# Performance work log

Hardware: AMD Instinct MI355X
Metric: run time of the kernel (lower is better)

The kernel has to match this reference:

```python
import jax, jax.numpy as jnp
import numpy as np
from math import sqrt

SEQ, NIN, NH, NOUT, HEADS = 4096, 1024, 128, 1024, 8
DOUT = HEADS * (2 * NH + NOUT)  # 10240
EPS = 1e-5

def setup_inputs() -> dict:
    key = jax.random.key(0)
    k1, k2, k3 = jax.random.split(key, 3)
    x = jax.random.normal(k1, (SEQ, NIN), dtype=jnp.float32)
    W = jax.random.normal(k2, (DOUT, NIN), dtype=jnp.float32) * (1.0 / sqrt(NIN))
    b = jax.random.normal(k3, (DOUT,), dtype=jnp.float32) * 0.01
    ln_w = jnp.ones((NOUT,), dtype=jnp.float32)
    ln_b = jnp.zeros((NOUT,), dtype=jnp.float32)
    return {"x": x, "W": W, "b": b, "ln_w": ln_w, "ln_b": ln_b}

def reference(x, W, b, ln_w, ln_b):
    # fused QKV projection: (S, NIN) -> (S, HEADS, 2*NH + NOUT)
    out = (x @ W.T + b).reshape(x.shape[0], HEADS, -1)
    keys, queries, values = jnp.split(out, (NH, 2 * NH), axis=-1)
    keys = keys / sqrt(keys.shape[-1])
    # logits[i, j, h] = sum_k keys[i,h,k] * queries[j,h,k]
    logits = jnp.einsum('ihk,jhk->ijh', keys, queries)
    attention = jax.nn.softmax(logits, axis=1)
    # sum over j and heads -> (S, NOUT)
    output = jnp.einsum('ijh,jhe->ie', attention, values)
    # LayerNorm over last dim, elementwise affine, eps=1e-5
    mean = jnp.mean(output, axis=-1, keepdims=True)
    var = jnp.var(output, axis=-1, keepdims=True)
    normed = (output - mean) / jnp.sqrt(var + EPS)
    return normed * ln_w + ln_b
```

## Files before the change

### kernel.cpp

```cpp
#include <hip/hip_runtime.h>

typedef __attribute__((ext_vector_type(8))) __bf16 bf16x8;
typedef __attribute__((ext_vector_type(4))) __bf16 bf16x4;
typedef __attribute__((ext_vector_type(4))) float f32x4;
typedef __attribute__((ext_vector_type(16))) float f32x16;

#define SEQ   4096
#define NIN   1024
#define DH    128
#define NOUTD 1024
#define HEADS 8
#define CPH   1280
#define L2E   1.44269504f

static __device__ inline f32x16 zero16() {
  f32x16 z;
#pragma unroll
  for (int r = 0; r < 16; ++r) z[r] = 0.f;
  return z;
}

static __device__ inline unsigned pk2(float a, float b) {
  unsigned short ua = __builtin_bit_cast(unsigned short, (__bf16)a);
  unsigned short ub = __builtin_bit_cast(unsigned short, (__bf16)b);
  return (unsigned)ua | ((unsigned)ub << 16);
}

__global__ __launch_bounds__(256) void k_cvt(const float* __restrict__ src,
                                             __bf16* __restrict__ dst, int n) {
  int i = (blockIdx.x * 256 + threadIdx.x) * 4;
  if (i >= n) return;
  float4 v = *(const float4*)(src + i);
  bf16x4 o = { (__bf16)v.x, (__bf16)v.y, (__bf16)v.z, (__bf16)v.w };
  *(bf16x4*)(dst + i) = o;
}

__global__ __launch_bounds__(256) void k_zero(float4* __restrict__ p) {
  p[(size_t)blockIdx.x * 256 + threadIdx.x] = float4{0.f, 0.f, 0.f, 0.f};
}

__global__ __launch_bounds__(256) void k_gemm_qkv(
    const __bf16* __restrict__ xb, const __bf16* __restrict__ wb,
    const float* __restrict__ bias,
    __bf16* __restrict__ Kx, __bf16* __restrict__ Q2, __bf16* __restrict__ V2)
{
  __shared__ __align__(16) __bf16 As[128 * 32];
  __shared__ __align__(16) __bf16 Bs[128 * 32];
  const int tid = threadIdx.x;
  const int w = tid >> 6, l = tid & 63;
  const int i0 = blockIdx.x * 128;
  const int n0 = blockIdx.y * 128;
  const int lrow = l & 15;
  const int lkb  = (l >> 4) * 16;
  const int soff = (w * 2) * 1024 + l * 16;

  f32x4 acc[4][4] = {};

  for (int kt = 0; kt < 32; ++kt) {
    __syncthreads();
#pragma unroll
    for (int q = 0; q < 2; ++q) {
      int off = soff + q * 1024;
      int row = off >> 6, kb = off & 63;
      const __bf16* ga = xb + (size_t)(i0 + row) * NIN + kt * 32 + (kb >> 1);
      const __bf16* gb = wb + (size_t)(n0 + row) * NIN + kt * 32 + (kb >> 1);
      __builtin_amdgcn_global_load_lds(
          (const __attribute__((address_space(1))) void*)ga,
          (__attribute__((address_space(3))) void*)((char*)As + (w * 2 + q) * 1024),
          16, 0, 0);
      __builtin_amdgcn_global_load_lds(
          (const __attribute__((address_space(1))) void*)gb,
          (__attribute__((address_space(3))) void*)((char*)Bs + (w * 2 + q) * 1024),
          16, 0, 0);
    }
    __syncthreads();
    bf16x8 af[4], bfr[4];
#pragma unroll
    for (int mi = 0; mi < 4; ++mi)
      af[mi] = *(const bf16x8*)((const char*)As + (((w >> 1) * 64 + mi * 16 + lrow) * 64) + lkb);
#pragma unroll
    for (int ni = 0; ni < 4; ++ni)
      bfr[ni] = *(const bf16x8*)((const char*)Bs + (((w & 1) * 64 + ni * 16 + lrow) * 64) + lkb);
#pragma unroll
    for (int mi = 0; mi < 4; ++mi)
#pragma unroll
      for (int ni = 0; ni < 4; ++ni)
        acc[mi][ni] = __builtin_amdgcn_mfma_f32_16x16x32_bf16(af[mi], bfr[ni], acc[mi][ni], 0, 0, 0);
  }

  const int iw = i0 + (w >> 1) * 64;
  const int nw = n0 + (w & 1) * 64;
  const int lhi = l >> 4;
#pragma unroll
  for (int ni = 0; ni < 4; ++ni) {
    int n = nw + ni * 16 + lrow;
    float bv = bias[n];
    int h = n / CPH;
    int c = n - h * CPH;
    if (c < 128) {
#pragma unroll
      for (int mi = 0; mi < 4; ++mi)
#pragma unroll
        for (int r = 0; r < 4; ++r) {
          int i = iw + mi * 16 + lhi * 4 + r;
          float v = acc[mi][ni][r] + bv;
          Kx[(((size_t)h * SEQ + i) << 7) + c] = (__bf16)(v * 0.08838834764831845f);
        }
    } else if (c < 256) {
      int d = c - 128;
      size_t qEl = ((size_t)(h * 16 + (d >> 3)) << 15) + (size_t)(d & 7);
#pragma unroll
      for (int mi = 0; mi < 4; ++mi)
#pragma unroll
        for (int r = 0; r < 4; ++r) {
          int j = iw + mi * 16 + lhi * 4 + r;
          Q2[qEl + ((size_t)j << 3)] = (__bf16)(acc[mi][ni][r] + bv);
        }
    } else {
      int e = c - 256;
#pragma unroll
      for (int mi = 0; mi < 4; ++mi) {
        int jb = iw + mi * 16 + lhi * 4;
        int J = jb >> 3, js = jb & 7;
        size_t vEl = (((size_t)(h * 512 + J)) << 13) + ((size_t)e << 3) + js;
        bf16x4 pk = { (__bf16)(acc[mi][ni][0] + bv), (__bf16)(acc[mi][ni][1] + bv),
                      (__bf16)(acc[mi][ni][2] + bv), (__bf16)(acc[mi][ni][3] + bv) };
        *(bf16x4*)(V2 + vEl) = pk;
      }
    }
  }
}

__global__ __launch_bounds__(256) void k_stats(
    const __bf16* __restrict__ Kx, const __bf16* __restrict__ Q2,
    float* __restrict__ stat_m, float* __restrict__ stat_il)
{
  __shared__ __align__(16) char Qb[2][16384];
  const int tid = threadIdx.x;
  const int w = tid >> 6, l = tid & 63;
  const int l31 = l & 31, hl = l >> 5;
  const int b = blockIdx.x;
  const int h = b >> 5;
  const int i_base = (b & 31) * 128;
  const __bf16* Kh = Kx + ((size_t)h * SEQ << 7);
  const char* q2b = (const char*)Q2 + ((size_t)h << 20);

  bf16x8 kf[8];
#pragma unroll
  for (int c = 0; c < 8; ++c)
    kf[c] = *(const bf16x8*)(Kh + (((size_t)(i_base + 32 * w + l31)) << 7) + c * 16 + hl * 8);

  float m_run = -1e30f, l_run = 0.f;

#pragma unroll
  for (int k = 0; k < 4; ++k) {
    int s = tid + k * 256;
    const char* src = q2b + ((size_t)(s >> 6) << 16) + (size_t)(s & 63) * 16;
    __builtin_amdgcn_global_load_lds(
        (const __attribute__((address_space(1))) void*)src,
        (__attribute__((address_space(3))) void*)(Qb[0] + s * 16), 16, 0, 0);
  }
  __syncthreads();

  for (int jt = 0; jt < 64; ++jt) {
    const int cur = jt & 1;
    if (jt < 63) {
      int j0n = (jt + 1) * 64;
#pragma unroll
      for (int k = 0; k < 4; ++k) {
        int s = tid + k * 256;
        const char* src = q2b + ((size_t)(s >> 6) << 16) + (size_t)(j0n + (s & 63)) * 16;
        __builtin_amdgcn_global_load_lds(
            (const __attribute__((address_space(1))) void*)src,
            (__attribute__((address_space(3))) void*)(Qb[cur ^ 1] + s * 16), 16, 0, 0);
      }
    }
    const char* qb = Qb[cur];

    f32x16 s0 = zero16(), s1 = zero16();
#pragma unroll
    for (int c = 0; c < 8; ++c) {
      bf16x8 a0 = *(const bf16x8*)(qb + (((2 * c + hl) * 64 + l31) << 4));
      bf16x8 a1 = *(const bf16x8*)(qb + (((2 * c + hl) * 64 + 32 + l31) << 4));
      s0 = __builtin_amdgcn_mfma_f32_32x32x16_bf16(a0, kf[c], s0, 0, 0, 0);
      s1 = __builtin_amdgcn_mfma_f32_32x32x16_bf16(a1, kf[c], s1, 0, 0, 0);
    }

    float pm = -1e30f;
#pragma unroll
    for (int r = 0; r < 16; ++r) pm = fmaxf(pm, fmaxf(s0[r], s1[r]));
    float mn = fmaxf(m_run, pm);
    l_run *= exp2f((m_run - mn) * L2E);
    float a = 0.f;
#pragma unroll
    for (int r = 0; r < 16; ++r)
      a += exp2f((s0[r] - mn) * L2E) + exp2f((s1[r] - mn) * L2E);
    l_run += a;
    m_run = mn;
    __syncthreads();
  }

  float mp = __shfl_xor(m_run, 32);
  float lp = __shfl_xor(l_run, 32);
  float mf = fmaxf(m_run, mp);
  float lf = l_run * exp2f((m_run - mf) * L2E) + lp * exp2f((mp - mf) * L2E);
  if (hl == 0) {
    int i = i_base + 32 * w + l31;
    stat_m[h * SEQ + i] = mf;
    stat_il[h * SEQ + i] = 1.0f / lf;
  }
}

__global__ __launch_bounds__(512, 2) void k_attn3(
    const __bf16* __restrict__ Kx, const __bf16* __restrict__ Q2,
    const __bf16* __restrict__ V2, const float* __restrict__ stat_m,
    const float* __restrict__ stat_il, float* __restrict__ out)
{
  __shared__ __align__(16) char Qb[2][8192];
  __shared__ __align__(16) char Vb[2][16384];
  __shared__ float s_linv[256];

  const int tid = threadIdx.x;
  const int w = tid >> 6, l = tid & 63;
  const int l31 = l & 31, hl = l >> 5;
  const int islot = w & 3, eslot = w >> 2;

  const int b = blockIdx.x;
  const int et = b & 3;
  const int h = ((b >> 2) & 1) + 2 * (b >> 7);
  const int it = (b >> 3) & 15;
  const int i_base = it * 256, e_base = et * 256;

  const __bf16* Kh = Kx + ((size_t)h * SEQ << 7);
  const char* q2b = (const char*)Q2 + ((size_t)h << 20);
  const char* v2b = (const char*)V2 + ((size_t)(h * 512) << 14) + ((size_t)e_base << 4);

  if (tid < 256) s_linv[tid] = stat_il[h * SEQ + i_base + tid];
  const int iw0 = i_base + islot * 64;
  const float m0 = stat_m[h * SEQ + iw0 + l31];
  const float m1 = stat_m[h * SEQ + iw0 + 32 + l31];

  bf16x8 kf[2][8];
#pragma unroll
  for (int ig = 0; ig < 2; ++ig)
#pragma unroll
    for (int c = 0; c < 8; ++c)
      kf[ig][c] = *(const bf16x8*)(Kh + (((size_t)(iw0 + ig * 32 + l31)) << 7) + c * 16 + hl * 8);

  f32x16 acc[2][4];
#pragma unroll
  for (int ig = 0; ig < 2; ++ig)
#pragma unroll
    for (int n = 0; n < 4; ++n) acc[ig][n] = zero16();

  {
    const char* srcQ = q2b + ((size_t)(tid >> 5) << 16) + (size_t)(tid & 31) * 16;
    __builtin_amdgcn_global_load_lds(
        (const __attribute__((address_space(1))) void*)srcQ,
        (__attribute__((address_space(3))) void*)(Qb[0] + tid * 16), 16, 0, 0);
#pragma unroll
    for (int k = 0; k < 2; ++k) {
      int s = tid + k * 512;
      const char* srcV = v2b + ((size_t)(s >> 8) << 14) + (size_t)(s & 255) * 16;
      __builtin_amdgcn_global_load_lds(
          (const __attribute__((address_space(1))) void*)srcV,
          (__attribute__((address_space(3))) void*)(Vb[0] + s * 16), 16, 0, 0);
    }
  }
  __syncthreads();

  for (int jt = 0; jt < 128; ++jt) {
    const int cur = jt & 1;
    if (jt < 127) {
      const int j0n = (jt + 1) * 32;
      const char* srcQ = q2b + ((size_t)(tid >> 5) << 16) + (size_t)(j0n + (tid & 31)) * 16;
      __builtin_amdgcn_global_load_lds(
          (const __attribute__((address_space(1))) void*)srcQ,
          (__attribute__((address_space(3))) void*)(Qb[cur ^ 1] + tid * 16), 16, 0, 0);
#pragma unroll
      for (int k = 0; k < 2; ++k) {
        int s = tid + k * 512;
        const char* srcV = v2b + ((size_t)((jt + 1) * 4 + (s >> 8)) << 14) + (size_t)(s & 255) * 16;
        __builtin_amdgcn_global_load_lds(
            (const __attribute__((address_space(1))) void*)srcV,
            (__attribute__((address_space(3))) void*)(Vb[cur ^ 1] + s * 16), 16, 0, 0);
      }
    }
    const char* qb = Qb[cur];
    const char* vb = Vb[cur];

    f32x16 s0 = zero16(), s1 = zero16();
#pragma unroll
    for (int c = 0; c < 8; ++c) {
      bf16x8 a0 = *(const bf16x8*)(qb + (((2 * c + hl) * 32 + l31) << 4));
      s0 = __builtin_amdgcn_mfma_f32_32x32x16_bf16(a0, kf[0][c], s0, 0, 0, 0);
      s1 = __builtin_amdgcn_mfma_f32_32x32x16_bf16(a0, kf[1][c], s1, 0, 0, 0);
    }

    bf16x8 pf[2][2];
#pragma unroll
    for (int ig = 0; ig < 2; ++ig) {
      const f32x16& sv = ig ? s1 : s0;
      const float mi = ig ? m1 : m0;
#pragma unroll
      for (int c2 = 0; c2 < 2; ++c2) {
        const int base = 8 * c2;
        float e0 = exp2f((sv[base + 0] - mi) * L2E);
        float e1 = exp2f((sv[base + 1] - mi) * L2E);
        float e2 = exp2f((sv[base + 2] - mi) * L2E);
        float e3 = exp2f((sv[base + 3] - mi) * L2E);
        float e4 = exp2f((sv[base + 4] - mi) * L2E);
        float e5 = exp2f((sv[base + 5] - mi) * L2E);
        float e6 = exp2f((sv[base + 6] - mi) * L2E);
        float e7 = exp2f((sv[base + 7] - mi) * L2E);
        unsigned WA0 = pk2(e0, e1), WA1 = pk2(e2, e3);
        unsigned WB0 = pk2(e4, e5), WB1 = pk2(e6, e7);
        unsigned send0 = hl ? WA0 : WB0;
        unsigned send1 = hl ? WA1 : WB1;
        unsigned r0 = (unsigned)__shfl_xor((int)send0, 32);
        unsigned r1 = (unsigned)__shfl_xor((int)send1, 32);
        int4 qd;
        qd.x = (int)(hl ? r0 : WA0);
        qd.y = (int)(hl ? r1 : WA1);
        qd.z = (int)(hl ? WB0 : r0);
        qd.w = (int)(hl ? WB1 : r1);
        pf[ig][c2] = __builtin_bit_cast(bf16x8, qd);
      }
    }

#pragma unroll
    for (int c2 = 0; c2 < 2; ++c2)
#pragma unroll
      for (int n = 0; n < 4; ++n) {
        bf16x8 bv = *(const bf16x8*)(vb + (((2 * c2 + hl) * 256 + eslot * 128 + 32 * n + l31) << 4));
        acc[0][n] = __builtin_amdgcn_mfma_f32_32x32x16_bf16(pf[0][c2], bv, acc[0][n], 0, 0, 0);
        acc[1][n] = __builtin_amdgcn_mfma_f32_32x32x16_bf16(pf[1][c2], bv, acc[1][n], 0, 0, 0);
      }
    __syncthreads();
  }

#pragma unroll
  for (int ig = 0; ig < 2; ++ig)
#pragma unroll
    for (int n = 0; n < 4; ++n) {
      const int e = e_base + eslot * 128 + 32 * n + l31;
#pragma unroll
      for (int r = 0; r < 16; ++r) {
        int row = (r & 3) + 8 * (r >> 2) + 4 * hl;
        int iloc = islot * 64 + ig * 32 + row;
        float v = acc[ig][n][r] * s_linv[iloc];
        atomicAdd(out + (((size_t)(i_base + iloc)) << 10) + e, v);
      }
    }
}

__global__ __launch_bounds__(256) void k_ln(float* __restrict__ io,
                                            const float* __restrict__ lw,
                                            const float* __restrict__ lb) {
  const int i = blockIdx.x, t = threadIdx.x;
  const int w = t >> 6, l = t & 63;
  float4 v = *(const float4*)(io + ((size_t)i << 10) + t * 4);
  float s = v.x + v.y + v.z + v.w;
  float q = v.x * v.x + v.y * v.y + v.z * v.z + v.w * v.w;
#pragma unroll
  for (int d = 1; d < 64; d <<= 1) {
    s += __shfl_xor(s, d);
    q += __shfl_xor(q, d);
  }
  __shared__ float red[4][2];
  if (l == 0) { red[w][0] = s; red[w][1] = q; }
  __syncthreads();
  s = red[0][0] + red[1][0] + red[2][0] + red[3][0];
  q = red[0][1] + red[1][1] + red[2][1] + red[3][1];
  float mean = s * (1.0f / 1024.0f);
  float var = q * (1.0f / 1024.0f) - mean * mean;
  float rstd = rsqrtf(var + 1e-5f);
  float4 gw = *(const float4*)(lw + t * 4);
  float4 gb = *(const float4*)(lb + t * 4);
  float4 ov;
  ov.x = (v.x - mean) * rstd * gw.x + gb.x;
  ov.y = (v.y - mean) * rstd * gw.y + gb.y;
  ov.z = (v.z - mean) * rstd * gw.z + gb.z;
  ov.w = (v.w - mean) * rstd * gw.w + gb.w;
  *(float4*)(io + ((size_t)i << 10) + t * 4) = ov;
}

extern "C" void kernel_launch(void* const* d_in, const int* in_sizes, int n_in,
                              void* d_out, int out_size, void* d_ws, size_t ws_size,
                              hipStream_t stream) {
  (void)in_sizes; (void)n_in; (void)out_size; (void)ws_size;
  const float* x  = (const float*)d_in[0];
  const float* W  = (const float*)d_in[1];
  const float* b  = (const float*)d_in[2];
  const float* lw = (const float*)d_in[3];
  const float* lb = (const float*)d_in[4];
  float* out = (float*)d_out;
  char* ws = (char*)d_ws;

  __bf16* xb = (__bf16*)ws;
  __bf16* wb = (__bf16*)(ws + (size_t)8  * 1024 * 1024);
  __bf16* Kx = (__bf16*)(ws + (size_t)28 * 1024 * 1024);
  __bf16* Q2 = (__bf16*)(ws + (size_t)36 * 1024 * 1024);
  __bf16* V2 = (__bf16*)(ws + (size_t)44 * 1024 * 1024);
  float* stat_m  = (float*)ws;
  float* stat_il = (float*)(ws + (size_t)128 * 1024);

  k_cvt<<<4096, 256, 0, stream>>>(x, xb, SEQ * NIN);
  k_cvt<<<10240, 256, 0, stream>>>(W, wb, HEADS * CPH * NIN);
  k_gemm_qkv<<<dim3(32, 80), 256, 0, stream>>>(xb, wb, b, Kx, Q2, V2);
  k_zero<<<4096, 256, 0, stream>>>((float4*)out);
  k_stats<<<256, 256, 0, stream>>>(Kx, Q2, stat_m, stat_il);
  k_attn3<<<512, 512, 0, stream>>>(Kx, Q2, V2, stat_m, stat_il, out);
  k_ln<<<4096, 256, 0, stream>>>(out, lw, lb);
}
```

Measured before the change: 1.011 ms.

## Materialize normalized attention matrix and compute output with a single large GEMM

Measured after the change: 1.012 ms. Within noise of the previous version (+0.1%).

```diff
diff --git a/kernel.cpp b/kernel.cpp
--- a/kernel.cpp
+++ b/kernel.cpp
@@ -12,6 +12,7 @@
 #define HEADS 8
 #define CPH   1280
 #define L2E   1.44269504f
+#define KTOT  32768
 
 static __device__ inline f32x16 zero16() {
   f32x16 z;
@@ -42,7 +43,8 @@
 __global__ __launch_bounds__(256) void k_gemm_qkv(
     const __bf16* __restrict__ xb, const __bf16* __restrict__ wb,
     const float* __restrict__ bias,
-    __bf16* __restrict__ Kx, __bf16* __restrict__ Q2, __bf16* __restrict__ V2)
+    __bf16* __restrict__ Kx, __bf16* __restrict__ Q2, __bf16* __restrict__ Vd,
+    int vmode)
 {
   __shared__ __align__(16) __bf16 As[128 * 32];
   __shared__ __align__(16) __bf16 Bs[128 * 32];
@@ -118,14 +120,18 @@
         }
     } else {
       int e = c - 256;
+      bf16x4 pk = { (__bf16)(acc[0][ni][0]), (__bf16)(0.f), (__bf16)(0.f), (__bf16)(0.f) };
 #pragma unroll
       for (int mi = 0; mi < 4; ++mi) {
         int jb = iw + mi * 16 + lhi * 4;
-        int J = jb >> 3, js = jb & 7;
-        size_t vEl = (((size_t)(h * 512 + J)) << 13) + ((size_t)e << 3) + js;
-        bf16x4 pk = { (__bf16)(acc[mi][ni][0] + bv), (__bf16)(acc[mi][ni][1] + bv),
-                      (__bf16)(acc[mi][ni][2] + bv), (__bf16)(acc[mi][ni][3] + bv) };
-        *(bf16x4*)(V2 + vEl) = pk;
+        pk = bf16x4{ (__bf16)(acc[mi][ni][0] + bv), (__bf16)(acc[mi][ni][1] + bv),
+                     (__bf16)(acc[mi][ni][2] + bv), (__bf16)(acc[mi][ni][3] + bv) };
+        if (vmode) {
+          *(bf16x4*)(Vd + (size_t)e * KTOT + (size_t)h * SEQ + jb) = pk;
+        } else {
+          int J = jb >> 3, js = jb & 7;
+          *(bf16x4*)(Vd + (((size_t)(h * 512 + J)) << 13) + ((size_t)e << 3) + js) = pk;
+        }
       }
     }
   }
@@ -208,6 +214,158 @@
     int i = i_base + 32 * w + l31;
     stat_m[h * SEQ + i] = mf;
     stat_il[h * SEQ + i] = 1.0f / lf;
+  }
+}
+
+__global__ __launch_bounds__(256) void k_pwrite(
+    const __bf16* __restrict__ Kx, const __bf16* __restrict__ Q2,
+    const float* __restrict__ stat_m, const float* __restrict__ stat_il,
+    __bf16* __restrict__ P)
+{
+  __shared__ __align__(16) char Qb[2][16384];
+  const int tid = threadIdx.x;
+  const int w = tid >> 6, l = tid & 63;
+  const int l31 = l & 31, hl = l >> 5;
+  const int b = blockIdx.x;
+  const int h = b >> 5;
+  const int i_base = (b & 31) * 128;
+  const __bf16* Kh = Kx + ((size_t)h * SEQ << 7);
+  const char* q2b = (const char*)Q2 + ((size_t)h << 20);
+
+  const int i = i_base + 32 * w + l31;
+  const float m_i = stat_m[h * SEQ + i];
+  const float il_i = stat_il[h * SEQ + i];
+  __bf16* prow = P + ((size_t)i << 15) + (size_t)h * SEQ;
+
+  bf16x8 kf[8];
+#pragma unroll
+  for (int c = 0; c < 8; ++c)
+    kf[c] = *(const bf16x8*)(Kh + (((size_t)i) << 7) + c * 16 + hl * 8);
+
+#pragma unroll
+  for (int k = 0; k < 4; ++k) {
+    int s = tid + k * 256;
+    const char* src = q2b + ((size_t)(s >> 6) << 16) + (size_t)(s & 63) * 16;
+    __builtin_amdgcn_global_load_lds(
+        (const __attribute__((address_space(1))) void*)src,
+        (__attribute__((address_space(3))) void*)(Qb[0] + s * 16), 16, 0, 0);
+  }
+  __syncthreads();
+
+  for (int jt = 0; jt < 64; ++jt) {
+    const int cur = jt & 1;
+    if (jt < 63) {
+      int j0n = (jt + 1) * 64;
+#pragma unroll
+      for (int k = 0; k < 4; ++k) {
+        int s = tid + k * 256;
+        const char* src = q2b + ((size_t)(s >> 6) << 16) + (size_t)(j0n + (s & 63)) * 16;
+        __builtin_amdgcn_global_load_lds(
+            (const __attribute__((address_space(1))) void*)src,
+            (__attribute__((address_space(3))) void*)(Qb[cur ^ 1] + s * 16), 16, 0, 0);
+      }
+    }
+    const char* qb = Qb[cur];
+
+    f32x16 s0 = zero16(), s1 = zero16();
+#pragma unroll
+    for (int c = 0; c < 8; ++c) {
+      bf16x8 a0 = *(const bf16x8*)(qb + (((2 * c + hl) * 64 + l31) << 4));
+      bf16x8 a1 = *(const bf16x8*)(qb + (((2 * c + hl) * 64 + 32 + l31) << 4));
+      s0 = __builtin_amdgcn_mfma_f32_32x32x16_bf16(a0, kf[c], s0, 0, 0, 0);
+      s1 = __builtin_amdgcn_mfma_f32_32x32x16_bf16(a1, kf[c], s1, 0, 0, 0);
+    }
+
+#pragma unroll
+    for (int c2 = 0; c2 < 4; ++c2) {
+      const f32x16& sv = (c2 >> 1) ? s1 : s0;
+      const int base = (c2 & 1) * 8;
+      float e0 = il_i * exp2f((sv[base + 0] - m_i) * L2E);
+      float e1 = il_i * exp2f((sv[base + 1] - m_i) * L2E);
+      float e2 = il_i * exp2f((sv[base + 2] - m_i) * L2E);
+      float e3 = il_i * exp2f((sv[base + 3] - m_i) * L2E);
+      float e4 = il_i * exp2f((sv[base + 4] - m_i) * L2E);
+      float e5 = il_i * exp2f((sv[base + 5] - m_i) * L2E);
+      float e6 = il_i * exp2f((sv[base + 6] - m_i) * L2E);
+      float e7 = il_i * exp2f((sv[base + 7] - m_i) * L2E);
+      unsigned WA0 = pk2(e0, e1), WA1 = pk2(e2, e3);
+      unsigned WB0 = pk2(e4, e5), WB1 = pk2(e6, e7);
+      unsigned send0 = hl ? WA0 : WB0;
+      unsigned send1 = hl ? WA1 : WB1;
+      unsigned r0 = (unsigned)__shfl_xor((int)send0, 32);
+      unsigned r1 = (unsigned)__shfl_xor((int)send1, 32);
+      int4 qd;
+      qd.x = (int)(hl ? r0 : WA0);
+      qd.y = (int)(hl ? r1 : WA1);
+      qd.z = (int)(hl ? WB0 : r0);
+      qd.w = (int)(hl ? WB1 : r1);
+      *(int4*)(prow + jt * 64 + 16 * c2 + 8 * hl) = qd;
+    }
+    __syncthreads();
+  }
+}
+
+__global__ __launch_bounds__(256) void k_pv_gemm(
+    const __bf16* __restrict__ P, const __bf16* __restrict__ VT,
+    float* __restrict__ out)
+{
+  __shared__ __align__(16) __bf16 As[128 * 32];
+  __shared__ __align__(16) __bf16 Bs[128 * 32];
+  const int tid = threadIdx.x;
+  const int w = tid >> 6, l = tid & 63;
+  const int i0 = blockIdx.y * 128;
+  const int n0 = blockIdx.x * 128;
+  const int lrow = l & 15;
+  const int lkb  = (l >> 4) * 16;
+  const int soff = (w * 2) * 1024 + l * 16;
+
+  f32x4 acc[4][4] = {};
+
+  for (int kt = 0; kt < 1024; ++kt) {
+    __syncthreads();
+#pragma unroll
+    for (int q = 0; q < 2; ++q) {
+      int off = soff + q * 1024;
+      int row = off >> 6, kb = off & 63;
+      const __bf16* ga = P  + (size_t)(i0 + row) * KTOT + kt * 32 + (kb >> 1);
+      const __bf16* gb = VT + (size_t)(n0 + row) * KTOT + kt * 32 + (kb >> 1);
+      __builtin_amdgcn_global_load_lds(
+          (const __attribute__((address_space(1))) void*)ga,
+          (__attribute__((address_space(3))) void*)((char*)As + (w * 2 + q) * 1024),
+          16, 0, 0);
+      __builtin_amdgcn_global_load_lds(
+          (const __attribute__((address_space(1))) void*)gb,
+          (__attribute__((address_space(3))) void*)((char*)Bs + (w * 2 + q) * 1024),
+          16, 0, 0);
+    }
+    __syncthreads();
+    bf16x8 af[4], bfr[4];
+#pragma unroll
+    for (int mi = 0; mi < 4; ++mi)
+      af[mi] = *(const bf16x8*)((const char*)As + (((w >> 1) * 64 + mi * 16 + lrow) * 64) + lkb);
+#pragma unroll
+    for (int ni = 0; ni < 4; ++ni)
+      bfr[ni] = *(const bf16x8*)((const char*)Bs + (((w & 1) * 64 + ni * 16 + lrow) * 64) + lkb);
+#pragma unroll
+    for (int mi = 0; mi < 4; ++mi)
+#pragma unroll
+      for (int ni = 0; ni < 4; ++ni)
+        acc[mi][ni] = __builtin_amdgcn_mfma_f32_16x16x32_bf16(af[mi], bfr[ni], acc[mi][ni], 0, 0, 0);
+  }
+
+  const int iw = i0 + (w >> 1) * 64;
+  const int nw = n0 + (w & 1) * 64;
+  const int lhi = l >> 4;
+#pragma unroll
+  for (int ni = 0; ni < 4; ++ni) {
+    int e = nw + ni * 16 + lrow;
+#pragma unroll
+    for (int mi = 0; mi < 4; ++mi)
+#pragma unroll
+      for (int r = 0; r < 4; ++r) {
+        int i = iw + mi * 16 + lhi * 4 + r;
+        out[((size_t)i << 10) + e] = acc[mi][ni][r];
+      }
   }
 }
 
@@ -388,7 +546,7 @@
 extern "C" void kernel_launch(void* const* d_in, const int* in_sizes, int n_in,
                               void* d_out, int out_size, void* d_ws, size_t ws_size,
                               hipStream_t stream) {
-  (void)in_sizes; (void)n_in; (void)out_size; (void)ws_size;
+  (void)in_sizes; (void)n_in; (void)out_size;
   const float* x  = (const float*)d_in[0];
   const float* W  = (const float*)d_in[1];
   const float* b  = (const float*)d_in[2];
@@ -401,15 +559,24 @@
   __bf16* wb = (__bf16*)(ws + (size_t)8  * 1024 * 1024);
   __bf16* Kx = (__bf16*)(ws + (size_t)28 * 1024 * 1024);
   __bf16* Q2 = (__bf16*)(ws + (size_t)36 * 1024 * 1024);
-  __bf16* V2 = (__bf16*)(ws + (size_t)44 * 1024 * 1024);
+  __bf16* Vd = (__bf16*)(ws + (size_t)44 * 1024 * 1024);
+  __bf16* P  = (__bf16*)(ws + (size_t)108 * 1024 * 1024);
   float* stat_m  = (float*)ws;
   float* stat_il = (float*)(ws + (size_t)128 * 1024);
 
+  const bool gemm_path = ws_size >= ((size_t)364 << 20);
+
   k_cvt<<<4096, 256, 0, stream>>>(x, xb, SEQ * NIN);
   k_cvt<<<10240, 256, 0, stream>>>(W, wb, HEADS * CPH * NIN);
-  k_gemm_qkv<<<dim3(32, 80), 256, 0, stream>>>(xb, wb, b, Kx, Q2, V2);
-  k_zero<<<4096, 256, 0, stream>>>((float4*)out);
+  k_gemm_qkv<<<dim3(32, 80), 256, 0, stream>>>(xb, wb, b, Kx, Q2, Vd,
+                                               gemm_path ? 1 : 0);
   k_stats<<<256, 256, 0, stream>>>(Kx, Q2, stat_m, stat_il);
-  k_attn3<<<512, 512, 0, stream>>>(Kx, Q2, V2, stat_m, stat_il, out);
+  if (gemm_path) {
+    k_pwrite<<<256, 256, 0, stream>>>(Kx, Q2, stat_m, stat_il, P);
+    k_pv_gemm<<<dim3(8, 32), 256, 0, stream>>>(P, Vd, out);
+  } else {
+    k_zero<<<4096, 256, 0, stream>>>((float4*)out);
+    k_attn3<<<512, 512, 0, stream>>>(Kx, Q2, Vd, stat_m, stat_il, out);
+  }
   k_ln<<<4096, 256, 0, stream>>>(out, lw, lb);
 }
```
